# Optimization experiments

Hardware: AMD Instinct MI355X
Metric: run time of the kernel (lower is better)

Reference implementation:

```python
import jax, jax.numpy as jnp
import numpy as np

B, S, D, E, TOP_K = 16, 2048, 240, 8, 2


def setup_inputs() -> dict:
    key = jax.random.key(0)
    k1, k2, k3 = jax.random.split(key, 3)
    scale = 1.0 / np.sqrt(D)
    return {
        "x": jax.random.normal(k1, (B, S, D), dtype=jnp.float32),
        "gate_w": jax.random.normal(k2, (E, D), dtype=jnp.float32) * scale,
        "gate_b": jnp.zeros((E,), dtype=jnp.float32),
        "expert_w": jax.random.normal(k3, (E, D, D), dtype=jnp.float32) * scale,
        "expert_b": jnp.zeros((E, D), dtype=jnp.float32),
    }


def reference(x, gate_w, gate_b, expert_w, expert_b):
    # Gating: softmax over experts, pick top-k, renormalize.
    logits = jnp.einsum("bsd,ed->bse", x, gate_w) + gate_b          # [B,S,E]
    gate_weights = jax.nn.softmax(logits, axis=-1)
    topk_w, topk_i = jax.lax.top_k(gate_weights, TOP_K)             # [B,S,K]
    topk_w = topk_w / jnp.sum(topk_w, axis=-1, keepdims=True)
    # Scatter renormalized top-k weights back to dense per-expert weights.
    onehot = jax.nn.one_hot(topk_i, E, dtype=x.dtype)               # [B,S,K,E]
    w_full = jnp.sum(topk_w[..., None] * onehot, axis=-2)           # [B,S,E]
    # Expert linears (torch Linear: y = x @ W^T + b), combined by gate weight.
    h = jnp.einsum("bsd,eod->bseo", x, expert_w) + expert_b         # [B,S,E,D]
    return jnp.einsum("bseo,bse->bso", h, w_full)                   # [B,S,D]
```

## Files before the change

kernel.cpp:

```cpp
#include <hip/hip_runtime.h>
#include <hip/hip_bf16.h>

#define TOKENS 32768
#define Dm 240
#define DP 256
#define NE 8
#define BK 32
#define NCHUNK 8
#define TILE_M 64
#define NB 64

typedef __bf16 bf16x8 __attribute__((ext_vector_type(8)));
typedef float  f32x4  __attribute__((ext_vector_type(4)));

__device__ __forceinline__ float b2f(unsigned short u) {
    union { unsigned int i; float f; } v; v.i = ((unsigned int)u) << 16; return v.f;
}
__device__ __forceinline__ float b2f_lo(unsigned u) {
    union { unsigned int i; float f; } v; v.i = u << 16; return v.f;
}
__device__ __forceinline__ float b2f_hi(unsigned u) {
    union { unsigned int i; float f; } v; v.i = u & 0xFFFF0000u; return v.f;
}
__device__ __forceinline__ unsigned short f2b(float f) {
    unsigned int i = __builtin_bit_cast(unsigned int, f);
    unsigned int r = (i + 0x7FFFu + ((i >> 16) & 1u)) >> 16;
    return (unsigned short)r;
}
__device__ __forceinline__ unsigned short f2h(float f) {
    _Float16 h = (_Float16)f;
    union { _Float16 h; unsigned short u; } v; v.h = h; return v.u;
}
__device__ __forceinline__ float h2f(unsigned short u) {
    union { _Float16 h; unsigned short u; } v; v.u = u; return (float)v.h;
}
__device__ __forceinline__ uint4 pack8(float4 a, float4 b) {
    union { unsigned short u[8]; uint4 v; } r;
    r.u[0] = f2b(a.x); r.u[1] = f2b(a.y); r.u[2] = f2b(a.z); r.u[3] = f2b(a.w);
    r.u[4] = f2b(b.x); r.u[5] = f2b(b.y); r.u[6] = f2b(b.z); r.u[7] = f2b(b.w);
    return r.v;
}

__device__ __forceinline__ void gload_lds16(const void* g, void* l) {
    __builtin_amdgcn_global_load_lds(
        (const __attribute__((address_space(1))) void*)g,
        (__attribute__((address_space(3))) void*)l,
        16, 0, 0);
}

__device__ __forceinline__ bool block_detect_f32(const unsigned short* x,
                                                 int tid, int* dh) {
    if (tid == 0) *dh = 0;
    __syncthreads();
    uint4 q = *(const uint4*)&x[tid * 8];
    unsigned w[4] = {q.x, q.y, q.z, q.w};
    int hits = 0;
    #pragma unroll
    for (int i = 0; i < 4; i++) {
        if ((((w[i] & 0xFFFFu) >> 7) & 0xFFu) >= 0xC0u) hits++;
        if ((((w[i] >> 16)      >> 7) & 0xFFu) >= 0xC0u) hits++;
    }
    if (hits) atomicAdd(dh, hits);
    __syncthreads();
    return *dh > 8;
}

__global__ __launch_bounds__(256) void wconv_kernel(
    const void* __restrict__ ewv, const void* __restrict__ ebv,
    const unsigned short* __restrict__ xus,
    int* __restrict__ flag, int* __restrict__ cnt,
    unsigned short* __restrict__ wpad, float* __restrict__ ebpad)
{
    __shared__ int dh;
    int tid = threadIdx.x;
    const bool f32 = block_detect_f32(xus, tid, &dh);
    if (blockIdx.x == 0) {
        if (tid == 0) flag[0] = f32 ? 1 : 0;
        if (tid < NB) cnt[tid] = 0;
    }

    int gidx = blockIdx.x * 256 + tid;

    if (gidx < NE * DP) {
        int e = gidx >> 8, n = gidx & 255;
        float bv = 0.f;
        if (n < Dm)
            bv = f32 ? ((const float*)ebv)[e * Dm + n]
                     : b2f(((const unsigned short*)ebv)[e * Dm + n]);
        ebpad[gidx] = bv;
    }

    int n = gidx & 255;
    int s = (gidx >> 8) & 3;
    int c = (gidx >> 10) & 7;
    int e = gidx >> 13;
    int k = c * 32 + s * 8;
    uint4 v = make_uint4(0, 0, 0, 0);
    if (n < Dm && k < Dm) {
        if (f32) {
            const float* src = (const float*)ewv + ((long)e * Dm + n) * Dm + k;
            v = pack8(*(const float4*)src, *(const float4*)(src + 4));
        } else {
            v = *(const uint4*)((const unsigned short*)ewv + ((long)e * Dm + n) * Dm + k);
        }
    }
    *(uint4*)&wpad[(long)gidx * 8] = v;
}

__global__ __launch_bounds__(256) void gate_kernel(
    const void* __restrict__ xv, const void* __restrict__ gwv,
    const void* __restrict__ gbv,
    int* __restrict__ cnt, unsigned* __restrict__ rt,
    unsigned short* __restrict__ xpad)
{
    __shared__ float gwsF[NE * Dm];
    __shared__ int h[NB];
    __shared__ int base[NB];
    __shared__ int dh;

    int tid = threadIdx.x;
    if (tid < NB) h[tid] = 0;
    const bool f32 = block_detect_f32((const unsigned short*)xv, tid, &dh);

    if (f32) {
        if (tid < 240) {
            const float* s = (const float*)gwv + tid * 8;
            float4 a = *(const float4*)s;
            float4 b4 = *(const float4*)(s + 4);
            float* d = &gwsF[tid * 8];
            *(float4*)d = a; *(float4*)(d + 4) = b4;
        }
    } else {
        if (tid < 240) {
            unsigned short* gb16 = (unsigned short*)gwsF;
            *(uint4*)&gb16[tid * 8] =
                *(const uint4*)((const unsigned short*)gwv + tid * 8);
        }
    }
    __syncthreads();

    int grp = tid >> 3;
    int j   = tid & 7;
    int t   = blockIdx.x * 32 + grp;

    float acc[NE] = {0.f, 0.f, 0.f, 0.f, 0.f, 0.f, 0.f, 0.f};
    unsigned short* xo = xpad + (long)t * DP;

    if (f32) {
        const float* xf = (const float*)xv + (long)t * Dm;
        #pragma unroll
        for (int i = 0; i < 4; i++) {
            int g = j + 8 * i;
            if (g < 30) {
                float4 xa = *(const float4*)&xf[g * 8];
                float4 xb = *(const float4*)&xf[g * 8 + 4];
                *(uint4*)&xo[g * 8] = pack8(xa, xb);
                #pragma unroll
                for (int e = 0; e < NE; e++) {
                    const float* gp = &gwsF[e * Dm + g * 8];
                    float4 ga = *(const float4*)gp;
                    float4 gc = *(const float4*)(gp + 4);
                    acc[e] += xa.x * ga.x + xa.y * ga.y + xa.z * ga.z + xa.w * ga.w
                            + xb.x * gc.x + xb.y * gc.y + xb.z * gc.z + xb.w * gc.w;
                }
            } else {
                *(uint4*)&xo[g * 8] = make_uint4(0, 0, 0, 0);
            }
        }
    } else {
        const unsigned short* xb = (const unsigned short*)xv + (long)t * Dm;
        const unsigned short* gb16 = (const unsigned short*)gwsF;
        #pragma unroll
        for (int i = 0; i < 4; i++) {
            int g = j + 8 * i;
            if (g < 30) {
                uint4 xq = *(const uint4*)&xb[g * 8];
                *(uint4*)&xo[g * 8] = xq;
                float x0 = b2f_lo(xq.x), x1 = b2f_hi(xq.x);
                float x2 = b2f_lo(xq.y), x3 = b2f_hi(xq.y);
                float x4 = b2f_lo(xq.z), x5 = b2f_hi(xq.z);
                float x6 = b2f_lo(xq.w), x7 = b2f_hi(xq.w);
                #pragma unroll
                for (int e = 0; e < NE; e++) {
                    uint4 gq = *(const uint4*)&gb16[e * Dm + g * 8];
                    acc[e] += x0 * b2f_lo(gq.x) + x1 * b2f_hi(gq.x)
                            + x2 * b2f_lo(gq.y) + x3 * b2f_hi(gq.y)
                            + x4 * b2f_lo(gq.z) + x5 * b2f_hi(gq.z)
                            + x6 * b2f_lo(gq.w) + x7 * b2f_hi(gq.w);
                }
            } else {
                *(uint4*)&xo[g * 8] = make_uint4(0, 0, 0, 0);
            }
        }
    }

    #pragma unroll
    for (int m = 1; m < 8; m <<= 1)
        #pragma unroll
        for (int e = 0; e < NE; e++)
            acc[e] += __shfl_xor(acc[e], m, 64);

    int bb = 0; float w0 = 0.f;
    if (j == 0) {
        #pragma unroll
        for (int e = 0; e < NE; e++)
            acc[e] += f32 ? ((const float*)gbv)[e]
                          : b2f(((const unsigned short*)gbv)[e]);
        float l0 = -1e30f; int e0 = 0;
        #pragma unroll
        for (int e = 0; e < NE; e++) if (acc[e] > l0) { l0 = acc[e]; e0 = e; }
        float l1 = -1e30f; int e1 = 0;
        #pragma unroll
        for (int e = 0; e < NE; e++) if (e != e0 && acc[e] > l1) { l1 = acc[e]; e1 = e; }
        w0 = 1.f / (1.f + __expf(l1 - l0));
        bb = e0 * 8 + e1;
        atomicAdd(&h[bb], 1);
    }
    __syncthreads();
    if (tid < NB) {
        int c = h[tid];
        if (c) base[tid] = atomicAdd(&cnt[tid], c);
        h[tid] = 0;
    }
    __syncthreads();
    if (j == 0) {
        int o = atomicAdd(&h[bb], 1);
        rt[bb * TOKENS + base[bb] + o] = ((unsigned)t << 16) | (unsigned)f2h(w0);
    }
}

__global__ __launch_bounds__(256, 2) void expert_kernel(
    const unsigned short* __restrict__ xp,
    const unsigned short* __restrict__ wp,
    const float* __restrict__ ebpad,
    const int* __restrict__ flag,
    const int* __restrict__ cnt, const unsigned* __restrict__ rt,
    void* __restrict__ outv)
{
    __shared__ __align__(16) unsigned short Xc[NCHUNK][4][64][8];
    __shared__ int cntS[NB];

    const bool f32o = (*flag != 0);
    int tid = threadIdx.x;
    if (tid < NB) cntS[tid] = cnt[tid];
    __syncthreads();

    int nwg = gridDim.x;
    int fid = blockIdx.x;
    if ((nwg & 7) == 0)
        fid = (blockIdx.x & 7) * (nwg >> 3) + (blockIdx.x >> 3);

    int b = -1, t = 0, accn = 0;
    for (int i = 0; i < NB; i++) {
        int ti = (cntS[i] + 63) >> 6;
        if (fid < accn + ti) { b = i; t = fid - accn; break; }
        accn += ti;
    }
    if (b < 0) return;
    int e0 = b >> 3, e1 = b & 7;
    int ne = cntS[b];
    int m0 = t * TILE_M;
    int rows = min(TILE_M, ne - m0);

    int lane = tid & 63;
    int wv   = tid >> 6;

    unsigned rvp = rt[b * TOKENS + min(m0 + lane, ne - 1)];
    int   tokL = (int)(rvp >> 16);
    float w0L  = h2f((unsigned short)(rvp & 0xFFFFu));

    const unsigned short* xsrc = xp + (long)tokL * DP + wv * 8;
    #pragma unroll
    for (int c = 0; c < NCHUNK; c++)
        gload_lds16(xsrc + c * BK, &Xc[c][wv][0][0]);
    __syncthreads();

    int frow = lane & 15;
    int slot = lane >> 4;
    const unsigned short* wb0 = wp + (long)e0 * 65536 + slot * 2048
                                   + (wv * 64 + frow) * 8;
    const unsigned short* wb1 = wp + (long)e1 * 65536 + slot * 2048
                                   + (wv * 64 + frow) * 8;

    f32x4 acc0[4][4] = {};
    f32x4 acc1[4][4] = {};

    #pragma unroll
    for (int c = 0; c < NCHUNK; c++) {
        bf16x8 a[4], b0[4], b1[4];
        #pragma unroll
        for (int mt = 0; mt < 4; mt++)
            a[mt] = *(const bf16x8*)&Xc[c][slot][mt * 16 + frow][0];
        #pragma unroll
        for (int nt = 0; nt < 4; nt++) {
            b0[nt] = *(const bf16x8*)&wb0[c * 8192 + nt * 128];
            b1[nt] = *(const bf16x8*)&wb1[c * 8192 + nt * 128];
        }
        #pragma unroll
        for (int nt = 0; nt < 4; nt++)
            #pragma unroll
            for (int mt = 0; mt < 4; mt++) {
                acc0[mt][nt] = __builtin_amdgcn_mfma_f32_16x16x32_bf16(
                    a[mt], b0[nt], acc0[mt][nt], 0, 0, 0);
                acc1[mt][nt] = __builtin_amdgcn_mfma_f32_16x16x32_bf16(
                    a[mt], b1[nt], acc1[mt][nt], 0, 0, 0);
            }
    }

    int colg = lane & 15;
    int rq   = (lane >> 4) << 2;
    float b0n[4], b1n[4];
    #pragma unroll
    for (int nt = 0; nt < 4; nt++) {
        int n = wv * 64 + nt * 16 + colg;
        b0n[nt] = ebpad[e0 * DP + n];
        b1n[nt] = ebpad[e1 * DP + n];
    }
    #pragma unroll
    for (int mt = 0; mt < 4; mt++) {
        #pragma unroll
        for (int r = 0; r < 4; r++) {
            int m = mt * 16 + rq + r;
            int   tok = __shfl(tokL, m);
            float w0  = __shfl(w0L, m);
            float w1  = 1.f - w0;
            if (m < rows) {
                #pragma unroll
                for (int nt = 0; nt < 4; nt++) {
                    int n = wv * 64 + nt * 16 + colg;
                    if (n < Dm) {
                        float val = (acc0[mt][nt][r] + b0n[nt]) * w0
                                  + (acc1[mt][nt][r] + b1n[nt]) * w1;
                        long idx = (long)tok * Dm + n;
                        if (f32o) ((float*)outv)[idx] = val;
                        else      ((unsigned short*)outv)[idx] = f2b(val);
                    }
                }
            }
        }
    }
}

__global__ void detect_kernel(const unsigned short* __restrict__ x, int* flag,
                              int* __restrict__ cnt) {
    int lane = threadIdx.x;
    cnt[lane] = 0;
    int hits = 0;
    for (int i = lane; i < 2048; i += 64) {
        unsigned e = (x[i] >> 7) & 0xFFu;
        if (e >= 0xC0u) hits++;
    }
    #pragma unroll
    for (int off = 32; off >= 1; off >>= 1) hits += __shfl_xor(hits, off, 64);
    if (lane == 0) flag[0] = (hits > 8) ? 1 : 0;
}

__global__ void init_kernel(int* cnt) {
    if (threadIdx.x < 16) cnt[threadIdx.x] = 0;
}

__global__ void zero_kernel(void* outv, const int* flag, int nelem) {
    long i = (long)blockIdx.x * blockDim.x + threadIdx.x;
    long stride = (long)gridDim.x * blockDim.x;
    if (*flag) {
        float* o = (float*)outv;
        for (; i < nelem; i += stride) o[i] = 0.f;
    } else {
        unsigned* o = (unsigned*)outv;
        long n = nelem >> 1;
        for (; i < n; i += stride) o[i] = 0u;
    }
}

template<bool FP32>
__global__ __launch_bounds__(256) void gate_fb_kernel(
    const void* __restrict__ xv, const void* __restrict__ gwv,
    const void* __restrict__ gbv, const int* __restrict__ flag,
    int* __restrict__ cnt, unsigned* __restrict__ rt, int cap)
{
    if ((*flag != 0) != FP32) return;
    __shared__ unsigned rv[256];
    __shared__ int h[16];
    __shared__ int base[16];

    int tid = threadIdx.x;
    if (tid < 16) h[tid] = 0;
    int t = blockIdx.x * 256 + tid;

    float acc[NE];
    #pragma unroll
    for (int e = 0; e < NE; e++)
        acc[e] = FP32 ? ((const float*)gbv)[e]
                      : b2f(((const unsigned short*)gbv)[e]);

    if (FP32) {
        const float* xf  = (const float*)xv + (long)t * Dm;
        const float* gwf = (const float*)gwv;
        for (int k = 0; k < Dm; k += 8) {
            float4 xa = *(const float4*)&xf[k];
            float4 xb = *(const float4*)&xf[k + 4];
            #pragma unroll
            for (int e = 0; e < NE; e++) {
                float4 ga = *(const float4*)&gwf[e * Dm + k];
                float4 gb = *(const float4*)&gwf[e * Dm + k + 4];
                acc[e] += xa.x * ga.x + xa.y * ga.y + xa.z * ga.z + xa.w * ga.w
                        + xb.x * gb.x + xb.y * gb.y + xb.z * gb.z + xb.w * gb.w;
            }
        }
    } else {
        const unsigned short* xb  = (const unsigned short*)xv + (long)t * Dm;
        const unsigned short* gwb = (const unsigned short*)gwv;
        for (int k = 0; k < Dm; k += 8) {
            uint4 xq = *(const uint4*)&xb[k];
            float x0 = b2f_lo(xq.x), x1 = b2f_hi(xq.x);
            float x2 = b2f_lo(xq.y), x3 = b2f_hi(xq.y);
            float x4 = b2f_lo(xq.z), x5 = b2f_hi(xq.z);
            float x6 = b2f_lo(xq.w), x7 = b2f_hi(xq.w);
            #pragma unroll
            for (int e = 0; e < NE; e++) {
                uint4 gq = *(const uint4*)&gwb[e * Dm + k];
                acc[e] += x0 * b2f_lo(gq.x) + x1 * b2f_hi(gq.x)
                        + x2 * b2f_lo(gq.y) + x3 * b2f_hi(gq.y)
                        + x4 * b2f_lo(gq.z) + x5 * b2f_hi(gq.z)
                        + x6 * b2f_lo(gq.w) + x7 * b2f_hi(gq.w);
            }
        }
    }

    float l0 = -1e30f; int e0 = 0;
    #pragma unroll
    for (int e = 0; e < NE; e++) if (acc[e] > l0) { l0 = acc[e]; e0 = e; }
    float l1 = -1e30f; int e1 = 0;
    #pragma unroll
    for (int e = 0; e < NE; e++) if (e != e0 && acc[e] > l1) { l1 = acc[e]; e1 = e; }
    float w0 = 1.f / (1.f + __expf(l1 - l0));

    rv[tid] = ((unsigned)e1 << 20) | ((unsigned)e0 << 16) | (unsigned)f2h(w0);
    __syncthreads();

    {
        unsigned v = rv[tid];
        atomicAdd(&h[(v >> 16) & 7], 1);
        atomicAdd(&h[8 + ((v >> 20) & 7)], 1);
    }
    __syncthreads();

    if (tid < 16) {
        base[tid] = atomicAdd(&cnt[tid], h[tid]);
        h[tid] = 0;
    }
    __syncthreads();

    {
        unsigned v = rv[tid];
        int tt = blockIdx.x * 256 + tid;
        int a0 = (v >> 16) & 7;
        int a1 = (v >> 20) & 7;
        unsigned short hw0 = (unsigned short)(v & 0xFFFFu);
        int o0 = atomicAdd(&h[a0], 1);
        int p0 = base[a0] + o0;
        if (p0 < cap) rt[a0 * cap + p0] = ((unsigned)tt << 16) | hw0;
        int o1 = atomicAdd(&h[8 + a1], 1);
        int p1 = base[8 + a1] + o1;
        if (p1 < cap) rt[(8 + a1) * cap + p1] = ((unsigned)tt << 16) | (unsigned)f2h(1.f - h2f(hw0));
    }
}

template<bool FP32>
__global__ __launch_bounds__(256) void expert_fb_kernel(
    const void* __restrict__ xv, const void* __restrict__ ewv,
    const void* __restrict__ ebv, const int* __restrict__ flag,
    const int* __restrict__ cnt, const unsigned* __restrict__ rt, int cap,
    void* __restrict__ outv, int slotBase, int accumulate)
{
    if ((*flag != 0) != FP32) return;
    int e = blockIdx.y;
    int tile = blockIdx.x;
    int bucket = slotBase + e;
    int ne = min(cnt[bucket], cap);
    int m0 = tile * TILE_M;
    if (m0 >= ne) return;
    int rows = min(TILE_M, ne - m0);

    __shared__ __align__(16) unsigned short Wcf[2][256][40];
    __shared__ __align__(16) unsigned short Xcf[2][TILE_M][40];
    __shared__ int   tokS[TILE_M];
    __shared__ float twS[TILE_M];

    int tid = threadIdx.x;
    if (tid < TILE_M) {
        int i = min(m0 + tid, ne - 1);
        unsigned v = rt[bucket * cap + i];
        tokS[tid] = (int)(v >> 16);
        twS[tid]  = (tid < rows) ? h2f((unsigned short)(v & 0xFFFFu)) : 0.f;
    }
    __syncthreads();

    int srow = tid >> 2;
    int part = tid & 3;

    auto stage = [&](int c, int buf) {
        int kk = c * BK + part * 8;
        bool kvalid = (kk < Dm);
        if (FP32) {
            const float* xf = (const float*)xv;
            const float* Wf = (const float*)ewv + e * Dm * Dm;
            uint4 xq = make_uint4(0, 0, 0, 0);
            if (kvalid) {
                const float* s = &xf[(long)tokS[srow] * Dm + kk];
                xq = pack8(*(const float4*)s, *(const float4*)(s + 4));
            }
            *(uint4*)&Xcf[buf][srow][part * 8] = xq;
            #pragma unroll
            for (int it = 0; it < 4; it++) {
                int n = srow + it * 64;
                uint4 wq = make_uint4(0, 0, 0, 0);
                if (kvalid && n < Dm) {
                    const float* s = &Wf[(long)n * Dm + kk];
                    wq = pack8(*(const float4*)s, *(const float4*)(s + 4));
                }
                *(uint4*)&Wcf[buf][n][part * 8] = wq;
            }
        } else {
            const unsigned short* xb = (const unsigned short*)xv;
            const unsigned short* Wb = (const unsigned short*)ewv + e * Dm * Dm;
            uint4 xq = make_uint4(0, 0, 0, 0);
            if (kvalid) xq = *(const uint4*)&xb[(long)tokS[srow] * Dm + kk];
            *(uint4*)&Xcf[buf][srow][part * 8] = xq;
            #pragma unroll
            for (int it = 0; it < 4; it++) {
                int n = srow + it * 64;
                uint4 wq = make_uint4(0, 0, 0, 0);
                if (kvalid && n < Dm) wq = *(const uint4*)&Wb[(long)n * Dm + kk];
                *(uint4*)&Wcf[buf][n][part * 8] = wq;
            }
        }
    };

    int lane = tid & 63;
    int wv   = tid >> 6;
    int frow = lane & 15;
    int koff = (lane >> 4) * 8;

    f32x4 acc[TILE_M / 16][4] = {};

    stage(0, 0);
    __syncthreads();
    for (int c = 0; c < NCHUNK; c++) {
        int buf = c & 1;
        bf16x8 a[TILE_M / 16], b[4];
        #pragma unroll
        for (int mt = 0; mt < TILE_M / 16; mt++)
            a[mt] = *(const bf16x8*)&Xcf[buf][mt * 16 + frow][koff];
        #pragma unroll
        for (int nt = 0; nt < 4; nt++)
            b[nt] = *(const bf16x8*)&Wcf[buf][wv * 64 + nt * 16 + frow][koff];
        if (c + 1 < NCHUNK) stage(c + 1, (c + 1) & 1);
        #pragma unroll
        for (int mt = 0; mt < TILE_M / 16; mt++)
            #pragma unroll
            for (int nt = 0; nt < 4; nt++)
                acc[mt][nt] = __builtin_amdgcn_mfma_f32_16x16x32_bf16(
                    a[mt], b[nt], acc[mt][nt], 0, 0, 0);
        __syncthreads();
    }

    int colg  = lane & 15;
    int rquad = (lane >> 4) * 4;
    #pragma unroll
    for (int nt = 0; nt < 4; nt++) {
        int n = wv * 64 + nt * 16 + colg;
        if (n >= Dm) continue;
        float bnv = FP32 ? ((const float*)ebv)[e * Dm + n]
                         : b2f(((const unsigned short*)ebv)[e * Dm + n]);
        #pragma unroll
        for (int mt = 0; mt < TILE_M / 16; mt++) {
            #pragma unroll
            for (int r = 0; r < 4; r++) {
                int m = mt * 16 + rquad + r;
                if (m < rows) {
                    float val = (acc[mt][nt][r] + bnv) * twS[m];
                    long idx = (long)tokS[m] * Dm + n;
                    if (FP32) {
                        float* o = (float*)outv + idx;
                        *o = accumulate ? (*o + val) : val;
                    } else {
                        unsigned short* o = (unsigned short*)outv + idx;
                        *o = accumulate ? f2b(b2f(*o) + val) : f2b(val);
                    }
                }
            }
        }
    }
}

extern "C" void kernel_launch(void* const* d_in, const int* in_sizes, int n_in,
                              void* d_out, int out_size, void* d_ws, size_t ws_size,
                              hipStream_t stream) {
    const void* x  = d_in[0];
    const void* gw = d_in[1];
    const void* gb = d_in[2];
    const void* ew = d_in[3];
    const void* eb = d_in[4];

    char* ws = (char*)d_ws;
    int* flag = (int*)ws;
    int* cnt  = (int*)(ws + 64);

    const size_t EB_OFF = 320;
    const size_t RT_OFF = EB_OFF + (size_t)NE * DP * 4;
    const size_t XP_OFF = RT_OFF + (size_t)NB * TOKENS * 4;
    const size_t WP_OFF = XP_OFF + (size_t)TOKENS * DP * 2;
    const size_t NEEDED = WP_OFF + (size_t)NE * NCHUNK * 8192 * 2;

    if (ws_size >= NEEDED) {
        float*          ebpad = (float*)(ws + EB_OFF);
        unsigned*       rt    = (unsigned*)(ws + RT_OFF);
        unsigned short* xpad  = (unsigned short*)(ws + XP_OFF);
        unsigned short* wpad  = (unsigned short*)(ws + WP_OFF);

        wconv_kernel<<<256, 256, 0, stream>>>(ew, eb, (const unsigned short*)x,
                                              flag, cnt, wpad, ebpad);
        gate_kernel<<<TOKENS / 32, 256, 0, stream>>>(x, gw, gb, cnt, rt, xpad);
        expert_kernel<<<TOKENS / TILE_M + NB, 256, 0, stream>>>(
            xpad, wpad, ebpad, flag, cnt, rt, d_out);
    } else {
        unsigned* rt = (unsigned*)(ws + 128);
        long capl = ((long)ws_size - 128) / (16 * sizeof(unsigned));
        if (capl > TOKENS) capl = TOKENS;
        if (capl < 64) capl = 64;
        int cap = (int)capl;
        int tiles = (cap + TILE_M - 1) / TILE_M;
        bool lossless = (cap >= TOKENS);
        int acc0 = lossless ? 0 : 1;

        detect_kernel<<<1, 64, 0, stream>>>((const unsigned short*)x, flag, cnt);
        init_kernel<<<1, 64, 0, stream>>>(cnt);
        gate_fb_kernel<false><<<TOKENS / 256, 256, 0, stream>>>(x, gw, gb, flag, cnt, rt, cap);
        gate_fb_kernel<true ><<<TOKENS / 256, 256, 0, stream>>>(x, gw, gb, flag, cnt, rt, cap);
        if (!lossless)
            zero_kernel<<<1024, 256, 0, stream>>>(d_out, flag, out_size);
        expert_fb_kernel<false><<<dim3(tiles, NE), 256, 0, stream>>>(x, ew, eb, flag, cnt, rt, cap, d_out, 0, acc0);
        expert_fb_kernel<true ><<<dim3(tiles, NE), 256, 0, stream>>>(x, ew, eb, flag, cnt, rt, cap, d_out, 0, acc0);
        expert_fb_kernel<false><<<dim3(tiles, NE), 256, 0, stream>>>(x, ew, eb, flag, cnt, rt, cap, d_out, 8, 1);
        expert_fb_kernel<true ><<<dim3(tiles, NE), 256, 0, stream>>>(x, ew, eb, flag, cnt, rt, cap, d_out, 8, 1);
    }
}
```

Baseline: 145.7 us.

## Pad expert counters to separate lines and split expert tile across 8 waves

The per-bucket atomic counters are spread out with a stride of 16 ints, and the gate blocks visit them in a rotated order, to cut atomic contention on shared cache lines. The expert kernel now runs 512 threads per block, so each of 8 waves computes 32 output columns instead of 64. X chunk staging is also redistributed so each wave loads one chunk. This lowers per-wave accumulator registers and adds waves per tile for latency hiding, at the cost of each wave issuing more redundant A-fragment LDS reads relative to its MFMA work.

```diff
diff --git a/kernel.cpp b/kernel.cpp
--- a/kernel.cpp
+++ b/kernel.cpp
@@ -9,6 +9,7 @@
 #define NCHUNK 8
 #define TILE_M 64
 #define NB 64
+#define CSTR 16
 
 typedef __bf16 bf16x8 __attribute__((ext_vector_type(8)));
 typedef float  f32x4  __attribute__((ext_vector_type(4)));
@@ -52,15 +53,17 @@
                                                  int tid, int* dh) {
     if (tid == 0) *dh = 0;
     __syncthreads();
-    uint4 q = *(const uint4*)&x[tid * 8];
-    unsigned w[4] = {q.x, q.y, q.z, q.w};
-    int hits = 0;
-    #pragma unroll
-    for (int i = 0; i < 4; i++) {
-        if ((((w[i] & 0xFFFFu) >> 7) & 0xFFu) >= 0xC0u) hits++;
-        if ((((w[i] >> 16)      >> 7) & 0xFFu) >= 0xC0u) hits++;
-    }
-    if (hits) atomicAdd(dh, hits);
+    if (tid < 256) {
+        uint4 q = *(const uint4*)&x[tid * 8];
+        unsigned w[4] = {q.x, q.y, q.z, q.w};
+        int hits = 0;
+        #pragma unroll
+        for (int i = 0; i < 4; i++) {
+            if ((((w[i] & 0xFFFFu) >> 7) & 0xFFu) >= 0xC0u) hits++;
+            if ((((w[i] >> 16)      >> 7) & 0xFFu) >= 0xC0u) hits++;
+        }
+        if (hits) atomicAdd(dh, hits);
+    }
     __syncthreads();
     return *dh > 8;
 }
@@ -76,7 +79,7 @@
     const bool f32 = block_detect_f32(xus, tid, &dh);
     if (blockIdx.x == 0) {
         if (tid == 0) flag[0] = f32 ? 1 : 0;
-        if (tid < NB) cnt[tid] = 0;
+        for (int i = tid; i < NB * CSTR; i += 256) cnt[i] = 0;
     }
 
     int gidx = blockIdx.x * 256 + tid;
@@ -218,9 +221,10 @@
     }
     __syncthreads();
     if (tid < NB) {
-        int c = h[tid];
-        if (c) base[tid] = atomicAdd(&cnt[tid], c);
-        h[tid] = 0;
+        int i = (tid + blockIdx.x) & (NB - 1);
+        int c = h[i];
+        if (c) base[i] = atomicAdd(&cnt[i * CSTR], c);
+        h[i] = 0;
     }
     __syncthreads();
     if (j == 0) {
@@ -229,7 +233,7 @@
     }
 }
 
-__global__ __launch_bounds__(256, 2) void expert_kernel(
+__global__ __launch_bounds__(512, 2) void expert_kernel(
     const unsigned short* __restrict__ xp,
     const unsigned short* __restrict__ wp,
     const float* __restrict__ ebpad,
@@ -242,7 +246,7 @@
 
     const bool f32o = (*flag != 0);
     int tid = threadIdx.x;
-    if (tid < NB) cntS[tid] = cnt[tid];
+    if (tid < NB) cntS[tid] = cnt[tid * CSTR];
     __syncthreads();
 
     int nwg = gridDim.x;
@@ -263,41 +267,41 @@
     int rows = min(TILE_M, ne - m0);
 
     int lane = tid & 63;
-    int wv   = tid >> 6;
+    int w    = tid >> 6;
 
     unsigned rvp = rt[b * TOKENS + min(m0 + lane, ne - 1)];
     int   tokL = (int)(rvp >> 16);
     float w0L  = h2f((unsigned short)(rvp & 0xFFFFu));
 
-    const unsigned short* xsrc = xp + (long)tokL * DP + wv * 8;
-    #pragma unroll
-    for (int c = 0; c < NCHUNK; c++)
-        gload_lds16(xsrc + c * BK, &Xc[c][wv][0][0]);
+    const unsigned short* xbase = xp + (long)tokL * DP;
+    #pragma unroll
+    for (int i = 0; i < 4; i++)
+        gload_lds16(xbase + w * BK + i * 8, &Xc[w][i][0][0]);
     __syncthreads();
 
     int frow = lane & 15;
     int slot = lane >> 4;
     const unsigned short* wb0 = wp + (long)e0 * 65536 + slot * 2048
-                                   + (wv * 64 + frow) * 8;
+                                   + (w * 32 + frow) * 8;
     const unsigned short* wb1 = wp + (long)e1 * 65536 + slot * 2048
-                                   + (wv * 64 + frow) * 8;
-
-    f32x4 acc0[4][4] = {};
-    f32x4 acc1[4][4] = {};
+                                   + (w * 32 + frow) * 8;
+
+    f32x4 acc0[4][2] = {};
+    f32x4 acc1[4][2] = {};
 
     #pragma unroll
     for (int c = 0; c < NCHUNK; c++) {
-        bf16x8 a[4], b0[4], b1[4];
+        bf16x8 a[4], b0[2], b1[2];
         #pragma unroll
         for (int mt = 0; mt < 4; mt++)
             a[mt] = *(const bf16x8*)&Xc[c][slot][mt * 16 + frow][0];
         #pragma unroll
-        for (int nt = 0; nt < 4; nt++) {
+        for (int nt = 0; nt < 2; nt++) {
             b0[nt] = *(const bf16x8*)&wb0[c * 8192 + nt * 128];
             b1[nt] = *(const bf16x8*)&wb1[c * 8192 + nt * 128];
         }
         #pragma unroll
-        for (int nt = 0; nt < 4; nt++)
+        for (int nt = 0; nt < 2; nt++)
             #pragma unroll
             for (int mt = 0; mt < 4; mt++) {
                 acc0[mt][nt] = __builtin_amdgcn_mfma_f32_16x16x32_bf16(
@@ -309,10 +313,10 @@
 
     int colg = lane & 15;
     int rq   = (lane >> 4) << 2;
-    float b0n[4], b1n[4];
-    #pragma unroll
-    for (int nt = 0; nt < 4; nt++) {
-        int n = wv * 64 + nt * 16 + colg;
+    float b0n[2], b1n[2];
+    #pragma unroll
+    for (int nt = 0; nt < 2; nt++) {
+        int n = w * 32 + nt * 16 + colg;
         b0n[nt] = ebpad[e0 * DP + n];
         b1n[nt] = ebpad[e1 * DP + n];
     }
@@ -326,8 +330,8 @@
             float w1  = 1.f - w0;
             if (m < rows) {
                 #pragma unroll
-                for (int nt = 0; nt < 4; nt++) {
-                    int n = wv * 64 + nt * 16 + colg;
+                for (int nt = 0; nt < 2; nt++) {
+                    int n = w * 32 + nt * 16 + colg;
                     if (n < Dm) {
                         float val = (acc0[mt][nt][r] + b0n[nt]) * w0
                                   + (acc1[mt][nt][r] + b1n[nt]) * w1;
@@ -607,7 +611,7 @@
     int* flag = (int*)ws;
     int* cnt  = (int*)(ws + 64);
 
-    const size_t EB_OFF = 320;
+    const size_t EB_OFF = 64 + (size_t)NB * CSTR * 4;
     const size_t RT_OFF = EB_OFF + (size_t)NE * DP * 4;
     const size_t XP_OFF = RT_OFF + (size_t)NB * TOKENS * 4;
     const size_t WP_OFF = XP_OFF + (size_t)TOKENS * DP * 2;
@@ -622,7 +626,7 @@
         wconv_kernel<<<256, 256, 0, stream>>>(ew, eb, (const unsigned short*)x,
                                               flag, cnt, wpad, ebpad);
         gate_kernel<<<TOKENS / 32, 256, 0, stream>>>(x, gw, gb, cnt, rt, xpad);
-        expert_kernel<<<TOKENS / TILE_M + NB, 256, 0, stream>>>(
+        expert_kernel<<<TOKENS / TILE_M + NB, 512, 0, stream>>>(
             xpad, wpad, ebpad, flag, cnt, rt, d_out);
     } else {
         unsigned* rt = (unsigned*)(ws + 128);
```

Measured after the change: 140.1 us. 1.04x faster.
